# Optimization experiments

Measured on AMD Instinct MI355X. Metric: run time of the kernel, lower is better.

The kernel has to match this reference:

```python
import jax, jax.numpy as jnp
import numpy as np
from jax import lax

GS, NB, NC = 7, 2, 20
CONF_THR = 0.2
IOU_THR = 0.5
IMG_W = IMG_H = 448.0


def _conv(x, w, b, stride=1):
    y = lax.conv_general_dilated(x, w, (stride, stride), ((1, 1), (1, 1)),
                                 dimension_numbers=('NCHW', 'OIHW', 'NCHW'))
    return y + b[None, :, None, None]


def _lrelu(x):
    return jnp.where(x >= 0, x, 0.1 * x)


def _head(features, w1, b1, w2, b2, w3, b3, w4, b4, fc1_w, fc1_b, fc2_w, fc2_b):
    x = _lrelu(_conv(features, w1, b1))            # [B,1024,14,14]
    x = _lrelu(_conv(x, w2, b2, stride=2))         # [B,1024,7,7]
    x = _lrelu(_conv(x, w3, b3))
    x = _lrelu(_conv(x, w4, b4))
    x = x.reshape(x.shape[0], -1)                  # NCHW flatten, matches torch .view
    x = _lrelu(x @ fc1_w + fc1_b)
    x = jax.nn.sigmoid(x @ fc2_w + fc2_b)
    return x.reshape(-1, GS, GS, 5 * NB + NC)      # [B, j, i, 30]


def _decode(out):
    # replicate loop order: i outer, j inner, k inner-most; outputs indexed [b, j, i, :]
    B = out.shape[0]
    cell = 1.0 / GS
    o = jnp.swapaxes(out, 1, 2)                    # [b, i, j, c]
    bx = o[..., :5 * NB].reshape(B, GS, GS, NB, 5)
    scores = bx[..., 4]                            # [B,i,j,k]
    idx = jnp.arange(GS, dtype=out.dtype)
    x0 = idx[None, :, None, None] * cell           # uses i
    y0 = idx[None, None, :, None] * cell           # uses j
    cx = bx[..., 0] * cell + x0
    cy = bx[..., 1] * cell + y0
    w, h = bx[..., 2], bx[..., 3]
    boxes = jnp.stack([cx - 0.5 * w, cy - 0.5 * h, cx + 0.5 * w, cy + 0.5 * h], -1)
    labels = o[..., 5 * NB:].reshape(B, GS * GS, NC)   # one label vec per cell, (i,j) order
    return boxes.reshape(B, -1, 4), scores.reshape(B, -1), labels


def _nms_keep(boxes, scores, valid):
    # greedy NMS over N=GS*GS*NB candidates; invalid candidates sorted last
    N = scores.shape[0]
    s = jnp.where(valid, scores, -1.0)
    order = jnp.argsort(-s)
    b = boxes[order]
    v = valid[order]
    x1, y1, x2, y2 = b[:, 0], b[:, 1], b[:, 2], b[:, 3]
    areas = (x2 - x1) * (y2 - y1)
    iw = jnp.clip(jnp.minimum(x2[:, None], x2[None, :]) - jnp.maximum(x1[:, None], x1[None, :]), 0)
    ih = jnp.clip(jnp.minimum(y2[:, None], y2[None, :]) - jnp.maximum(y1[:, None], y1[None, :]), 0)
    inter = iw * ih
    iou = inter / (areas[:, None] + areas[None, :] - inter)
    later = jnp.arange(N)

    def body(i, state):
        suppressed, keep = state
        ki = v[i] & ~suppressed[i]
        suppressed = jnp.where(ki, suppressed | ((iou[i] > IOU_THR) & (later > i)), suppressed)
        keep = keep.at[i].set(ki)
        return suppressed, keep

    _, keep = lax.fori_loop(0, N, body, (jnp.zeros(N, bool), jnp.zeros(N, bool)))
    return jnp.zeros(N, bool).at[order].set(keep)


def setup_inputs() -> dict:
    key = jax.random.key(0)
    ks = jax.random.split(key, 8)
    B = 16
    d = {
        'features': jax.random.normal(ks[0], (B, 2048, 14, 14), jnp.float32),
        'w1': jax.random.normal(ks[1], (1024, 2048, 3, 3), jnp.float32) * 0.01,
        'b1': jnp.zeros((1024,), jnp.float32),
        'w2': jax.random.normal(ks[2], (1024, 1024, 3, 3), jnp.float32) * 0.01,
        'b2': jnp.zeros((1024,), jnp.float32),
        'w3': jax.random.normal(ks[3], (1024, 1024, 3, 3), jnp.float32) * 0.01,
        'b3': jnp.zeros((1024,), jnp.float32),
        'w4': jax.random.normal(ks[4], (1024, 1024, 3, 3), jnp.float32) * 0.01,
        'b4': jnp.zeros((1024,), jnp.float32),
        'fc1_w': jax.random.normal(ks[5], (50176, 4096), jnp.float32) * 0.004,
        'fc1_b': jnp.zeros((4096,), jnp.float32),
        'fc2_w': jax.random.normal(ks[6], (4096, GS * GS * (5 * NB + NC)), jnp.float32) * 0.02,
        'fc2_b': jnp.zeros((GS * GS * (5 * NB + NC),), jnp.float32),
    }
    return d


def reference(features, w1, b1, w2, b2, w3, b3, w4, b4, fc1_w, fc1_b, fc2_w, fc2_b):
    out = _head(features, w1, b1, w2, b2, w3, b3, w4, b4, fc1_w, fc1_b, fc2_w, fc2_b)
    boxes, scores, labels = _decode(out)           # [B,98,4],[B,98],[B,49,20]
    valid = scores >= CONF_THR                     # 'if proba < 0.2: continue' with proba=score*1.0
    keep = jax.vmap(_nms_keep)(boxes, scores, valid)  # [B,98] bool
    boxes_px = jnp.where(keep[..., None], boxes * IMG_W, 0.0)
    scores_k = jnp.where(keep, scores, 0.0)
    return boxes_px, scores_k, keep, labels
```

## Files before the change

kernel.cpp:

```cpp
#include <hip/hip_runtime.h>
#include <cstddef>

#define CONF_THR 0.2f
#define IOU_THR  0.5f
#define IMG_SZ   448.0f

typedef __attribute__((ext_vector_type(8))) _Float16 half8;
typedef __attribute__((ext_vector_type(4))) float f32x4;
typedef unsigned short u16;
typedef unsigned int   u32;

__device__ __forceinline__ u16 f2h(float x) {
    _Float16 h = (_Float16)x;
    return __builtin_bit_cast(u16, h);
}
__device__ __forceinline__ float h2f(u16 b) {
    _Float16 h = __builtin_bit_cast(_Float16, b);
    return (float)h;
}

#define GLOAD_LDS16(gsrc, ldst)                                              \
    __builtin_amdgcn_global_load_lds(                                        \
        (const __attribute__((address_space(1))) void*)(gsrc),               \
        (__attribute__((address_space(3))) void*)(ldst), 16, 0, 0)

__global__ __launch_bounds__(256)
void pad_split(const float* __restrict__ x, u16* __restrict__ xp,
               const int Cin, const int H, const int W,
               const int PW, const int PHW, const long PS)
{
    __shared__ float lds[64][200];
    const int t  = threadIdx.x;
    const int b  = blockIdx.x >> 5;
    const int cc = blockIdx.x & 31;
    const int ci0 = cc * 64;
    const int HW = H * W;

    for (int r = 0; r < 64; ++r) {
        for (int i = t; i < HW; i += 256)
            lds[r][i] = x[((long)b * Cin + ci0 + r) * HW + i];
    }
    __syncthreads();

    const int lci = t & 63;
    const int lp  = t >> 6;
    for (int pp = 0; pp < PHW / 4; ++pp) {
        const int pix = pp * 4 + lp;
        const int py = pix / PW, px = pix % PW;
        float v = 0.f;
        if (py >= 1 && py <= H && px >= 1 && px <= W)
            v = lds[lci][(py - 1) * W + (px - 1)];
        v *= 16.0f;
        u16 h = f2h(v);
        u16 m = f2h(v - h2f(h));
        const long off = ((long)b * PHW + pix) * Cin + ci0 + lci;
        xp[off] = h; xp[PS + off] = m;
    }
}

__global__ __launch_bounds__(256)
void wsplit_kernel(const float* __restrict__ w, u16* __restrict__ wT, int Cin)
{
    __shared__ float ws_l[2304];
    const int t  = threadIdx.x;
    const int cb = blockIdx.x;
    const int co = blockIdx.y;
    const long base = ((long)co * Cin + cb * 256) * 9;
    for (int i = t; i < 2304; i += 256) ws_l[i] = w[base + i];
    __syncthreads();
    const int ci = cb * 256 + t;
    const long PS = (long)9 * 1024 * Cin;
    #pragma unroll
    for (int tap = 0; tap < 9; ++tap) {
        float v = ws_l[t * 9 + tap] * 256.0f;
        u16 h = f2h(v);
        u16 m = f2h(v - h2f(h));
        long off = ((long)tap * 1024 + co) * Cin + ci;
        wT[off] = h; wT[PS + off] = m;
    }
}

template<int STRIDE>
__global__ __launch_bounds__(512, 4)
void conv_mfma(const u16* __restrict__ xp, const u16* __restrict__ wT,
               float* __restrict__ partial,
               const int Cin, const int PW, const int PHW,
               const int Wout, const int Ntot,
               const int sppsh, const int steps_pb, const int Npad,
               const long PSx)
{
    __shared__ u16 Alds[256 * 64];
    __shared__ u16 Blds[128 * 64];

    const int t  = threadIdx.x;

    const int gx = gridDim.x, gy = gridDim.y;
    const int nwg = gx * gy * gridDim.z;
    const int bid = blockIdx.x + gx * (blockIdx.y + gy * blockIdx.z);
    const int cpx = nwg >> 3;
    const int swz = (bid & 7) * cpx + (bid >> 3);
    const int bx  = swz % gx;
    const int rem = swz / gx;
    const int by  = rem % gy;
    const int bz  = rem / gy;

    const int m0 = bx * 256;
    const int n0 = by * 128;
    const int g0 = bz * steps_pb;
    const int HWout = Wout * Wout;

    int bpix[2], bblk[2];
    #pragma unroll
    for (int c = 0; c < 2; ++c) {
        const int idx = c * 512 + t;
        const int col = idx >> 3;
        const int blk = idx & 7;
        int n = n0 + col; if (n >= Ntot) n = 0;
        const int b  = n / HWout;
        const int rp = n - b * HWout;
        const int oy = rp / Wout;
        const int ox = rp - oy * Wout;
        bpix[c] = b * PHW + oy * STRIDE * PW + ox * STRIDE;
        bblk[c] = (blk ^ (col & 7)) * 8;
    }
    const int arow = t >> 3;
    const int ablk = ((t & 7) ^ (arow & 7)) * 8;
    const int wbase = (t & 448) * 16;

    const int wid = t >> 6, l = t & 63;
    const int wm = wid >> 1, wn = wid & 1;
    const int l16 = l & 15, lhi = l >> 4;

    const f32x4 zero4 = {0.f, 0.f, 0.f, 0.f};
    f32x4 acc[4][4];
    #pragma unroll
    for (int i = 0; i < 4; ++i)
        #pragma unroll
        for (int j = 0; j < 4; ++j) acc[i][j] = zero4;

    for (int s = 0; s < steps_pb; ++s) {
        const int g     = g0 + s;
        const int phase = g >> sppsh;
        const int cs    = g - (phase << sppsh);
        const int pair  = phase / 9;
        const int tap   = phase - pair * 9;
        const int pA = (0x100 >> (pair * 4)) & 15;
        const int pB = (0x010 >> (pair * 4)) & 15;
        const int ci0 = cs * 64;
        const int tapoff = (tap / 3) * PW + (tap % 3);

        const u16* Ag = wT + ((long)(pA * 9 + tap) * 1024 + m0) * Cin + ci0 + ablk;
        #pragma unroll
        for (int c = 0; c < 4; ++c)
            GLOAD_LDS16(Ag + (long)(c * 64 + arow) * Cin,
                        (char*)Alds + c * 8192 + wbase);
        const u16* Bg = xp + (long)pB * PSx + (long)tapoff * Cin + ci0;
        #pragma unroll
        for (int c = 0; c < 2; ++c)
            GLOAD_LDS16(Bg + (long)bpix[c] * Cin + bblk[c],
                        (char*)Blds + c * 8192 + wbase);

        __syncthreads();

        #pragma unroll
        for (int j = 0; j < 2; ++j) {
            const int kb = j * 64 + lhi * 16;
            half8 af[4], bf[4];
            #pragma unroll
            for (int f = 0; f < 4; ++f) {
                const int row = wm * 64 + f * 16 + l16;
                af[f] = *(const half8*)((const char*)Alds + row * 128
                                        + (kb ^ ((row & 7) << 4)));
            }
            #pragma unroll
            for (int f = 0; f < 4; ++f) {
                const int cc = wn * 64 + f * 16 + l16;
                bf[f] = *(const half8*)((const char*)Blds + cc * 128
                                        + (kb ^ ((cc & 7) << 4)));
            }
            #pragma unroll
            for (int fm = 0; fm < 4; ++fm)
                #pragma unroll
                for (int fn = 0; fn < 4; ++fn)
                    acc[fm][fn] = __builtin_amdgcn_mfma_f32_16x16x32_f16(
                        af[fm], bf[fn], acc[fm][fn], 0, 0, 0);
        }
        __syncthreads();
    }

    const long pbase = (long)bz * 1024;
    #pragma unroll
    for (int fm = 0; fm < 4; ++fm) {
        #pragma unroll
        for (int r = 0; r < 4; ++r) {
            const long mrow = pbase + m0 + wm * 64 + fm * 16 + lhi * 4 + r;
            float* prow = partial + mrow * Npad + n0 + wn * 64 + l16;
            #pragma unroll
            for (int fn = 0; fn < 4; ++fn)
                prow[fn * 16] = acc[fm][fn][r];
        }
    }
}

__global__ __launch_bounds__(256)
void reduce_nhwc(const float* __restrict__ partial, const float* __restrict__ bias,
                 u16* __restrict__ yp,
                 const int S, const int Npad, const int Ntot,
                 const int Wout, const int PW, const int PHW, const long PSy)
{
    __shared__ float lds[64][65];
    const int t  = threadIdx.x;
    const int m0 = blockIdx.x * 64;
    const int n0 = blockIdx.y * 64;
    const int HWout = Wout * Wout;

    const int lm = t >> 6, ln = t & 63;
    for (int r = 0; r < 16; ++r) {
        const int m = r * 4 + lm;
        const int n = n0 + ln;
        float v = 0.f;
        if (n < Ntot) {
            for (int s = 0; s < S; ++s)
                v += partial[((long)s * 1024 + m0 + m) * Npad + n];
            v = v * (1.0f / 4096.0f) + bias[m0 + m];
            v = (v >= 0.f) ? v : 0.1f * v;
        }
        lds[m][ln] = v;
    }
    __syncthreads();

    const int wn_ = t >> 6, wci = t & 63;
    for (int r = 0; r < 16; ++r) {
        const int pr = r * 4 + wn_;
        const int nn = n0 + pr;
        if (nn < Ntot) {
            const int b = nn / HWout;
            const int p = nn - b * HWout;
            const int py = p / Wout + 1, px = p % Wout + 1;
            const long off = ((long)b * PHW + py * PW + px) * 1024 + m0 + wci;
            const float vs = lds[wci][pr] * 16.0f;
            u16 h = f2h(vs);
            u16 m = f2h(vs - h2f(h));
            yp[off] = h; yp[PSy + off] = m;
        }
    }
}

__global__ __launch_bounds__(256)
void reduce_f32(const float* __restrict__ partial, const float* __restrict__ bias,
                float* __restrict__ yf,
                const int S, const int Npad, const int Ntot, const int HWout)
{
    const long idx = (long)blockIdx.x * 256 + threadIdx.x;
    if (idx >= (long)1024 * Ntot) return;
    const int m = (int)(idx / Ntot);
    const int n = (int)(idx - (long)m * Ntot);
    float v = 0.f;
    for (int s = 0; s < S; ++s)
        v += partial[((long)s * 1024 + m) * Npad + n];
    v = v * (1.0f / 4096.0f) + bias[m];
    v = (v >= 0.f) ? v : 0.1f * v;
    const int b = n / HWout, pix = n - b * HWout;
    yf[((long)b * 1024 + m) * HWout + pix] = v;
}

__global__ __launch_bounds__(256)
void fc1_partial(const float* __restrict__ x, const float* __restrict__ w,
                 float* __restrict__ part)
{
    __shared__ float xs[512][16];
    const int tid = threadIdx.x;
    const int n   = blockIdx.x * 1024 + tid * 4;
    const int kc  = blockIdx.y;
    const int k0  = kc * 512;

    for (int i = tid; i < 512 * 16; i += 256) {
        const int j = i >> 4;
        const int b = i & 15;
        xs[j][b] = x[(size_t)b * 50176 + k0 + j];
    }
    __syncthreads();

    f32x4 acc[16];
    #pragma unroll
    for (int b = 0; b < 16; ++b) acc[b] = (f32x4){0.f, 0.f, 0.f, 0.f};

    for (int j = 0; j < 512; ++j) {
        const f32x4 wv = *(const f32x4*)&w[(size_t)(k0 + j) * 4096 + n];
        #pragma unroll
        for (int b = 0; b < 16; ++b) {
            const float xb = xs[j][b];
            #pragma unroll
            for (int c = 0; c < 4; ++c)
                acc[b][c] = fmaf(xb, wv[c], acc[b][c]);
        }
    }

    #pragma unroll
    for (int b = 0; b < 16; ++b)
        *(f32x4*)&part[((size_t)kc * 16 + b) * 4096 + n] = acc[b];
}

__global__ __launch_bounds__(256)
void fc1_reduce(const float* __restrict__ part, const float* __restrict__ bias,
                float* __restrict__ y)
{
    const int i = blockIdx.x * 256 + threadIdx.x;
    float s = 0.f;
    for (int kc = 0; kc < 98; ++kc) s += part[(size_t)kc * 65536 + i];
    s += bias[i & 4095];
    y[i] = (s >= 0.f) ? s : 0.1f * s;
}

__global__ __launch_bounds__(256)
void fc2_partial(const float* __restrict__ x, const float* __restrict__ w,
                 float* __restrict__ part)
{
    __shared__ float xs[128][16];
    const int tid = threadIdx.x;
    const int n   = blockIdx.x * 256 + tid;
    const int kc  = blockIdx.y;
    const int k0  = kc * 128;

    for (int i = tid; i < 128 * 16; i += 256) {
        const int j = i >> 4;
        const int b = i & 15;
        xs[j][b] = x[(size_t)b * 4096 + k0 + j];
    }
    __syncthreads();

    float acc[16] = {};
    if (n < 1470) {
        for (int j = 0; j < 128; ++j) {
            const float wv = w[(size_t)(k0 + j) * 1470 + n];
            #pragma unroll
            for (int b4 = 0; b4 < 4; ++b4) {
                const float4 xv = *(const float4*)&xs[j][b4 * 4];
                acc[b4*4+0] = fmaf(xv.x, wv, acc[b4*4+0]);
                acc[b4*4+1] = fmaf(xv.y, wv, acc[b4*4+1]);
                acc[b4*4+2] = fmaf(xv.z, wv, acc[b4*4+2]);
                acc[b4*4+3] = fmaf(xv.w, wv, acc[b4*4+3]);
            }
        }
        #pragma unroll
        for (int b = 0; b < 16; ++b)
            part[((size_t)kc * 16 + b) * 1470 + n] = acc[b];
    }
}

__global__ __launch_bounds__(256)
void fc2_reduce(const float* __restrict__ part, const float* __restrict__ bias,
                float* __restrict__ y)
{
    const int i = blockIdx.x * 256 + threadIdx.x;
    if (i >= 16 * 1470) return;
    float s = 0.f;
    for (int kc = 0; kc < 32; ++kc) s += part[(size_t)kc * 23520 + i];
    const int n = i % 1470;
    s += bias[n];
    y[i] = 1.0f / (1.0f + expf(-s));
}

__global__ __launch_bounds__(128)
void decode_nms(const float* __restrict__ out2, float* __restrict__ dout)
{
    const int b = blockIdx.x;
    const int t = threadIdx.x;
    const float cell = 1.0f / 7.0f;
    const float* o = out2 + (size_t)b * 1470;

    __shared__ float bx[98][4];
    __shared__ float sc[98];
    __shared__ float area[98];
    __shared__ int   order[98];
    __shared__ int   rankof[98];
    __shared__ int   supp[98];
    __shared__ int   keep_s[98];

    if (t < 98) {
        const int gA = t / 14;
        const int r  = t % 14;
        const int gB = r >> 1;
        const int nb = r & 1;
        const int base = gB * 210 + gA * 30 + nb * 5;
        const float v0 = o[base + 0];
        const float v1 = o[base + 1];
        const float w  = o[base + 2];
        const float h  = o[base + 3];
        const float s  = o[base + 4];
        const float cx = v0 * cell + (float)gA * cell;
        const float cy = v1 * cell + (float)gB * cell;
        const float x1 = cx - 0.5f * w;
        const float y1 = cy - 0.5f * h;
        const float x2 = cx + 0.5f * w;
        const float y2 = cy + 0.5f * h;
        bx[t][0] = x1; bx[t][1] = y1; bx[t][2] = x2; bx[t][3] = y2;
        sc[t] = s;
        area[t] = (x2 - x1) * (y2 - y1);
        supp[t] = 0;
        keep_s[t] = 0;
    }
    __syncthreads();

    if (t < 98) {
        const float si = (sc[t] >= CONF_THR) ? sc[t] : -1.0f;
        int rank = 0;
        for (int j = 0; j < 98; ++j) {
            const float sj = (sc[j] >= CONF_THR) ? sc[j] : -1.0f;
            rank += (sj > si) || (sj == si && j < t);
        }
        order[rank] = t;
        rankof[t] = rank;
    }
    __syncthreads();

    for (int i = 0; i < 98; ++i) {
        const int oi = order[i];
        const bool ki = (sc[oi] >= CONF_THR) && (supp[i] == 0);
        if (t == 0) keep_s[i] = ki ? 1 : 0;
        if (ki && t < 98 && t > i) {
            const int oj = order[t];
            const float xx1 = fmaxf(bx[oi][0], bx[oj][0]);
            const float yy1 = fmaxf(bx[oi][1], bx[oj][1]);
            const float xx2 = fminf(bx[oi][2], bx[oj][2]);
            const float yy2 = fminf(bx[oi][3], bx[oj][3]);
            const float iw = fmaxf(xx2 - xx1, 0.f);
            const float ih = fmaxf(yy2 - yy1, 0.f);
            const float inter = iw * ih;
            const float iou = inter / (area[oi] + area[oj] - inter);
            if (iou > IOU_THR) supp[t] = 1;
        }
        __syncthreads();
    }

    float* out_boxes  = dout;
    float* out_scores = dout + 6272;
    float* out_keep   = dout + 7840;
    float* out_labels = dout + 9408;

    if (t < 98) {
        const bool kp = keep_s[rankof[t]] != 0;
        const size_t bi = ((size_t)b * 98 + t) * 4;
        out_boxes[bi + 0] = kp ? bx[t][0] * IMG_SZ : 0.f;
        out_boxes[bi + 1] = kp ? bx[t][1] * IMG_SZ : 0.f;
        out_boxes[bi + 2] = kp ? bx[t][2] * IMG_SZ : 0.f;
        out_boxes[bi + 3] = kp ? bx[t][3] * IMG_SZ : 0.f;
        out_scores[(size_t)b * 98 + t] = kp ? sc[t] : 0.f;
        out_keep[(size_t)b * 98 + t]   = kp ? 1.f : 0.f;
    }
    for (int i = t; i < 49 * 20; i += 128) {
        const int g  = i / 20;
        const int c  = i - g * 20;
        const int gA = g / 7;
        const int gB = g - gA * 7;
        out_labels[(size_t)b * 980 + i] = o[gB * 210 + gA * 30 + 10 + c];
    }
}

extern "C" void kernel_launch(void* const* d_in, const int* in_sizes, int n_in,
                              void* d_out, int out_size, void* d_ws, size_t ws_size,
                              hipStream_t stream)
{
    (void)in_sizes; (void)n_in; (void)out_size; (void)ws_size;

    const float* features = (const float*)d_in[0];
    const float* w1 = (const float*)d_in[1];
    const float* b1 = (const float*)d_in[2];
    const float* w2 = (const float*)d_in[3];
    const float* b2 = (const float*)d_in[4];
    const float* w3 = (const float*)d_in[5];
    const float* b3 = (const float*)d_in[6];
    const float* w4 = (const float*)d_in[7];
    const float* b4 = (const float*)d_in[8];
    const float* fc1_w = (const float*)d_in[9];
    const float* fc1_b = (const float*)d_in[10];
    const float* fc2_w = (const float*)d_in[11];
    const float* fc2_b = (const float*)d_in[12];

    char* W = (char*)d_ws;
    size_t o = 0;
    auto alloc = [&](size_t bytes) -> char* {
        char* r = W + o; o += (bytes + 255) & ~(size_t)255; return r;
    };
    u16*   wT      = (u16*)  alloc(75497472ULL);
    u16*   xp      = (u16*)  alloc(33554432ULL);
    u16*   actA    = (u16*)  alloc(16777216ULL);
    float* a4      = (float*)alloc(3211264ULL);
    float* partial = (float*)alloc(58720256ULL);
    float* fc1o    = (float*)alloc(262144ULL);
    float* part2   = (float*)alloc(3010560ULL);
    float* fc2o    = (float*)alloc(94080ULL);
    (void)alloc(4096);
    float* part1 = (float*)xp;
    u16*   actB  = (u16*)(xp + (24u << 20) / 2);

    const long PSxp = 8388608L;
    const long PSa  = 4194304L;
    const long PSb  = 1327104L;

    pad_split<<<512, 256, 0, stream>>>(features, xp, 2048, 14, 14, 16, 256, PSxp);

    wsplit_kernel<<<dim3(8, 1024), 256, 0, stream>>>(w1, wT, 2048);
    hipMemsetAsync(actA, 0, 16777216ULL, stream);
    conv_mfma<1><<<dim3(4, 25, 4), 512, 0, stream>>>(
        xp, wT, partial, 2048, 16, 256, 14, 3136, 5, 216, 3200, PSxp);
    hipMemsetAsync(actB, 0, 5308416ULL, stream);
    reduce_nhwc<<<dim3(16, 49), 256, 0, stream>>>(partial, b1, actA,
                                                  4, 3200, 3136, 14, 16, 256, PSa);

    wsplit_kernel<<<dim3(4, 1024), 256, 0, stream>>>(w2, wT, 1024);
    conv_mfma<2><<<dim3(4, 7, 16), 512, 0, stream>>>(
        actA, wT, partial, 1024, 16, 256, 7, 784, 4, 27, 896, PSa);
    reduce_nhwc<<<dim3(16, 13), 256, 0, stream>>>(partial, b2, actB,
                                                  16, 896, 784, 7, 9, 81, PSb);

    wsplit_kernel<<<dim3(4, 1024), 256, 0, stream>>>(w3, wT, 1024);
    conv_mfma<1><<<dim3(4, 7, 16), 512, 0, stream>>>(
        actB, wT, partial, 1024, 9, 81, 7, 784, 4, 27, 896, PSb);
    reduce_nhwc<<<dim3(16, 13), 256, 0, stream>>>(partial, b3, actB,
                                                  16, 896, 784, 7, 9, 81, PSb);

    wsplit_kernel<<<dim3(4, 1024), 256, 0, stream>>>(w4, wT, 1024);
    conv_mfma<1><<<dim3(4, 7, 16), 512, 0, stream>>>(
        actB, wT, partial, 1024, 9, 81, 7, 784, 4, 27, 896, PSb);
    reduce_f32<<<3136, 256, 0, stream>>>(partial, b4, a4, 16, 896, 784, 49);

    fc1_partial<<<dim3(4, 98), 256, 0, stream>>>(a4, fc1_w, part1);
    fc1_reduce<<<256, 256, 0, stream>>>(part1, fc1_b, fc1o);

    fc2_partial<<<dim3(6, 32), 256, 0, stream>>>(fc1o, fc2_w, part2);
    fc2_reduce<<<92, 256, 0, stream>>>(part2, fc2_b, fc2o);

    decode_nms<<<16, 128, 0, stream>>>(fc2o, (float*)d_out);
}
```

Baseline: 1.088 ms.

## Double-buffer conv MFMA LDS tiles and enlarge N tile to 256

```diff
diff --git a/kernel.cpp b/kernel.cpp
--- a/kernel.cpp
+++ b/kernel.cpp
@@ -81,7 +81,7 @@
 }
 
 template<int STRIDE>
-__global__ __launch_bounds__(512, 4)
+__global__ __launch_bounds__(512, 2)
 void conv_mfma(const u16* __restrict__ xp, const u16* __restrict__ wT,
                float* __restrict__ partial,
                const int Cin, const int PW, const int PHW,
@@ -89,10 +89,10 @@
                const int sppsh, const int steps_pb, const int Npad,
                const long PSx)
 {
-    __shared__ u16 Alds[256 * 64];
-    __shared__ u16 Blds[128 * 64];
-
-    const int t  = threadIdx.x;
+    __shared__ u16 Alds[2][256 * 64];
+    __shared__ u16 Blds[2][256 * 64];
+
+    const int t = threadIdx.x;
 
     const int gx = gridDim.x, gy = gridDim.y;
     const int nwg = gx * gy * gridDim.z;
@@ -105,13 +105,13 @@
     const int bz  = rem / gy;
 
     const int m0 = bx * 256;
-    const int n0 = by * 128;
+    const int n0 = by * 256;
     const int g0 = bz * steps_pb;
     const int HWout = Wout * Wout;
 
-    int bpix[2], bblk[2];
+    int bpix[4], bblk[4];
     #pragma unroll
-    for (int c = 0; c < 2; ++c) {
+    for (int c = 0; c < 4; ++c) {
         const int idx = c * 512 + t;
         const int col = idx >> 3;
         const int blk = idx & 7;
@@ -128,72 +128,91 @@
     const int wbase = (t & 448) * 16;
 
     const int wid = t >> 6, l = t & 63;
-    const int wm = wid >> 1, wn = wid & 1;
+    const int wm = wid >> 2, wn = wid & 3;
     const int l16 = l & 15, lhi = l >> 4;
 
     const f32x4 zero4 = {0.f, 0.f, 0.f, 0.f};
-    f32x4 acc[4][4];
+    f32x4 acc[8][4];
     #pragma unroll
-    for (int i = 0; i < 4; ++i)
+    for (int i = 0; i < 8; ++i)
         #pragma unroll
         for (int j = 0; j < 4; ++j) acc[i][j] = zero4;
 
+    const u16 *Aptr_n, *Bptr_n;
+#define DECODE(g) {                                                          \
+    const int phase_ = (g) >> sppsh; const int cs_ = (g) - (phase_ << sppsh);\
+    const int pair_ = phase_ / 9; const int tap_ = phase_ - pair_ * 9;       \
+    const int pA_ = (0x100 >> (pair_ * 4)) & 15;                  \
+    const int pB_ = (0x010 >> (pair_ * 4)) & 15;                  \
+    const int ci0_ = cs_ * 64;                                               \
+    const int tapoff_ = (tap_ / 3) * PW + (tap_ % 3);                        \
+    Aptr_n = wT + ((long)(pA_ * 9 + tap_) * 1024 + m0) * Cin + ci0_ + ablk;  \
+    Bptr_n = xp + (long)pB_ * PSx + (long)tapoff_ * Cin + ci0_; }
+
+#define STAGE_A(buf, c) GLOAD_LDS16(Aptr_n + (long)((c) * 64 + arow) * Cin,  \
+                                    (char*)Alds[buf] + (c) * 8192 + wbase)
+#define STAGE_B(buf, c) GLOAD_LDS16(Bptr_n + (long)bpix[c] * Cin + bblk[c],  \
+                                    (char*)Blds[buf] + (c) * 8192 + wbase)
+
+#define LOADB(buf, J)                                                        \
+    _Pragma("unroll")                                                        \
+    for (int f = 0; f < 4; ++f) {                                            \
+        const int cc = wn * 64 + f * 16 + l16;                               \
+        bfr[f] = *(const half8*)((const char*)Blds[buf] + cc * 128           \
+                                 + (((J) * 64 + lhi * 16) ^ ((cc & 7) << 4)));}
+
+#define PHASE(buf, J, H) {                                                   \
+    half8 af[4];                                                             \
+    _Pragma("unroll")                                                        \
+    for (int f = 0; f < 4; ++f) {                                            \
+        const int row = wm * 128 + ((H) * 4 + f) * 16 + l16;                 \
+        af[f] = *(const half8*)((const char*)Alds[buf] + row * 128           \
+                                + (((J) * 64 + lhi * 16) ^ ((row & 7) << 4)));}\
+    __builtin_amdgcn_s_setprio(1);                                           \
+    _Pragma("unroll")                                                        \
+    for (int fm = 0; fm < 4; ++fm)                                           \
+        _Pragma("unroll")                                                    \
+        for (int fn = 0; fn < 4; ++fn)                                       \
+            acc[(H) * 4 + fm][fn] = __builtin_amdgcn_mfma_f32_16x16x32_f16(  \
+                af[fm], bfr[fn], acc[(H) * 4 + fm][fn], 0, 0, 0);            \
+    __builtin_amdgcn_s_setprio(0); }
+
+    DECODE(g0);
+    STAGE_A(0, 0); STAGE_A(0, 1); STAGE_A(0, 2); STAGE_A(0, 3);
+    STAGE_B(0, 0); STAGE_B(0, 1); STAGE_B(0, 2); STAGE_B(0, 3);
+    __syncthreads();
+
     for (int s = 0; s < steps_pb; ++s) {
-        const int g     = g0 + s;
-        const int phase = g >> sppsh;
-        const int cs    = g - (phase << sppsh);
-        const int pair  = phase / 9;
-        const int tap   = phase - pair * 9;
-        const int pA = (0x100 >> (pair * 4)) & 15;
-        const int pB = (0x010 >> (pair * 4)) & 15;
-        const int ci0 = cs * 64;
-        const int tapoff = (tap / 3) * PW + (tap % 3);
-
-        const u16* Ag = wT + ((long)(pA * 9 + tap) * 1024 + m0) * Cin + ci0 + ablk;
-        #pragma unroll
-        for (int c = 0; c < 4; ++c)
-            GLOAD_LDS16(Ag + (long)(c * 64 + arow) * Cin,
-                        (char*)Alds + c * 8192 + wbase);
-        const u16* Bg = xp + (long)pB * PSx + (long)tapoff * Cin + ci0;
-        #pragma unroll
-        for (int c = 0; c < 2; ++c)
-            GLOAD_LDS16(Bg + (long)bpix[c] * Cin + bblk[c],
-                        (char*)Blds + c * 8192 + wbase);
-
+        const int cur = s & 1, nxt = cur ^ 1;
+        const bool more = (s + 1) < steps_pb;
+        if (more) { DECODE(g0 + s + 1); STAGE_A(nxt, 0); STAGE_A(nxt, 1); }
+        {
+            half8 bfr[4];
+            LOADB(cur, 0);
+            PHASE(cur, 0, 0);
+            if (more) { STAGE_A(nxt, 2); STAGE_A(nxt, 3); }
+            PHASE(cur, 0, 1);
+            if (more) { STAGE_B(nxt, 0); STAGE_B(nxt, 1); }
+            LOADB(cur, 1);
+            PHASE(cur, 1, 0);
+            if (more) { STAGE_B(nxt, 2); STAGE_B(nxt, 3); }
+            PHASE(cur, 1, 1);
+        }
         __syncthreads();
-
-        #pragma unroll
-        for (int j = 0; j < 2; ++j) {
-            const int kb = j * 64 + lhi * 16;
-            half8 af[4], bf[4];
-            #pragma unroll
-            for (int f = 0; f < 4; ++f) {
-                const int row = wm * 64 + f * 16 + l16;
-                af[f] = *(const half8*)((const char*)Alds + row * 128
-                                        + (kb ^ ((row & 7) << 4)));
-            }
-            #pragma unroll
-            for (int f = 0; f < 4; ++f) {
-                const int cc = wn * 64 + f * 16 + l16;
-                bf[f] = *(const half8*)((const char*)Blds + cc * 128
-                                        + (kb ^ ((cc & 7) << 4)));
-            }
-            #pragma unroll
-            for (int fm = 0; fm < 4; ++fm)
-                #pragma unroll
-                for (int fn = 0; fn < 4; ++fn)
-                    acc[fm][fn] = __builtin_amdgcn_mfma_f32_16x16x32_f16(
-                        af[fm], bf[fn], acc[fm][fn], 0, 0, 0);
-        }
-        __syncthreads();
-    }
+    }
+
+#undef DECODE
+#undef STAGE_A
+#undef STAGE_B
+#undef LOADB
+#undef PHASE
 
     const long pbase = (long)bz * 1024;
     #pragma unroll
-    for (int fm = 0; fm < 4; ++fm) {
+    for (int fm = 0; fm < 8; ++fm) {
         #pragma unroll
         for (int r = 0; r < 4; ++r) {
-            const long mrow = pbase + m0 + wm * 64 + fm * 16 + lhi * 4 + r;
+            const long mrow = pbase + m0 + wm * 128 + fm * 16 + lhi * 4 + r;
             float* prow = partial + mrow * Npad + n0 + wn * 64 + l16;
             #pragma unroll
             for (int fn = 0; fn < 4; ++fn)
@@ -486,7 +505,7 @@
     u16*   xp      = (u16*)  alloc(33554432ULL);
     u16*   actA    = (u16*)  alloc(16777216ULL);
     float* a4      = (float*)alloc(3211264ULL);
-    float* partial = (float*)alloc(58720256ULL);
+    float* partial = (float*)alloc(71303168ULL);
     float* fc1o    = (float*)alloc(262144ULL);
     float* part2   = (float*)alloc(3010560ULL);
     float* fc2o    = (float*)alloc(94080ULL);
@@ -502,28 +521,28 @@
 
     wsplit_kernel<<<dim3(8, 1024), 256, 0, stream>>>(w1, wT, 2048);
     hipMemsetAsync(actA, 0, 16777216ULL, stream);
-    conv_mfma<1><<<dim3(4, 25, 4), 512, 0, stream>>>(
-        xp, wT, partial, 2048, 16, 256, 14, 3136, 5, 216, 3200, PSxp);
+    conv_mfma<1><<<dim3(4, 13, 4), 512, 0, stream>>>(
+        xp, wT, partial, 2048, 16, 256, 14, 3136, 5, 216, 3328, PSxp);
     hipMemsetAsync(actB, 0, 5308416ULL, stream);
     reduce_nhwc<<<dim3(16, 49), 256, 0, stream>>>(partial, b1, actA,
-                                                  4, 3200, 3136, 14, 16, 256, PSa);
+                                                  4, 3328, 3136, 14, 16, 256, PSa);
 
     wsplit_kernel<<<dim3(4, 1024), 256, 0, stream>>>(w2, wT, 1024);
-    conv_mfma<2><<<dim3(4, 7, 16), 512, 0, stream>>>(
-        actA, wT, partial, 1024, 16, 256, 7, 784, 4, 27, 896, PSa);
+    conv_mfma<2><<<dim3(4, 4, 16), 512, 0, stream>>>(
+        actA, wT, partial, 1024, 16, 256, 7, 784, 4, 27, 1024, PSa);
     reduce_nhwc<<<dim3(16, 13), 256, 0, stream>>>(partial, b2, actB,
-                                                  16, 896, 784, 7, 9, 81, PSb);
+                                                  16, 1024, 784, 7, 9, 81, PSb);
 
     wsplit_kernel<<<dim3(4, 1024), 256, 0, stream>>>(w3, wT, 1024);
-    conv_mfma<1><<<dim3(4, 7, 16), 512, 0, stream>>>(
-        actB, wT, partial, 1024, 9, 81, 7, 784, 4, 27, 896, PSb);
+    conv_mfma<1><<<dim3(4, 4, 16), 512, 0, stream>>>(
+        actB, wT, partial, 1024, 9, 81, 7, 784, 4, 27, 1024, PSb);
     reduce_nhwc<<<dim3(16, 13), 256, 0, stream>>>(partial, b3, actB,
-                                                  16, 896, 784, 7, 9, 81, PSb);
+                                                  16, 1024, 784, 7, 9, 81, PSb);
 
     wsplit_kernel<<<dim3(4, 1024), 256, 0, stream>>>(w4, wT, 1024);
-    conv_mfma<1><<<dim3(4, 7, 16), 512, 0, stream>>>(
-        actB, wT, partial, 1024, 9, 81, 7, 784, 4, 27, 896, PSb);
-    reduce_f32<<<3136, 256, 0, stream>>>(partial, b4, a4, 16, 896, 784, 49);
+    conv_mfma<1><<<dim3(4, 4, 16), 512, 0, stream>>>(
+        actB, wT, partial, 1024, 9, 81, 7, 784, 4, 27, 1024, PSb);
+    reduce_f32<<<3136, 256, 0, stream>>>(partial, b4, a4, 16, 1024, 784, 49);
 
     fc1_partial<<<dim3(4, 98), 256, 0, stream>>>(a4, fc1_w, part1);
     fc1_reduce<<<256, 256, 0, stream>>>(part1, fc1_b, fc1o);
```

Result: slower. 1.326 ms (+21.9%).
